# Kernel tuning notes

Measured on AMD Instinct MI355X. Metric: run time of the kernel, lower is better.

The kernel has to match this reference:

```python
import jax, jax.numpy as jnp
import numpy as np

EMBED_CHOICES = (512, 768, 1024)
RATIO_CHOICES = (2, 3, 4)
D_MAX = 1024           # max embed_dim
H_MAX = 4096           # max expansion dim = 1024 * 4


def setup_inputs() -> dict:
    key = jax.random.key(0)
    ks = jax.random.split(key, 7)
    return {
        "x": jax.random.normal(ks[0], (8, 512, D_MAX), dtype=jnp.float32),
        "w0": jax.random.normal(ks[1], (H_MAX, D_MAX), dtype=jnp.float32) * 0.02,
        "b0": jax.random.normal(ks[2], (H_MAX,), dtype=jnp.float32) * 0.02,
        "w1": jax.random.normal(ks[3], (D_MAX, H_MAX), dtype=jnp.float32) * 0.02,
        "b1": jax.random.normal(ks[4], (D_MAX,), dtype=jnp.float32) * 0.02,
        "arch_embed": jax.random.normal(ks[5], (3,), dtype=jnp.float32),
        "arch_mlp": jax.random.normal(ks[6], (3,), dtype=jnp.float32),
    }


def _effective_masks(a, b):
    """Weighted-sum-of-sliced-linears == single linear with masked effective weights.

    Candidate (e, r): uses W0[:e*r, :e] on x[..., :e], zero-padded to H_MAX,
    and W1[:e, :e*r] on h[..., :e*r], zero-padded to D_MAX.
    """
    col = jnp.arange(D_MAX)
    row = jnp.arange(H_MAX)
    m0 = jnp.zeros((H_MAX, D_MAX), dtype=jnp.float32)
    bm0 = jnp.zeros((H_MAX,), dtype=jnp.float32)
    m1 = jnp.zeros((D_MAX, H_MAX), dtype=jnp.float32)
    bm1 = jnp.zeros((D_MAX,), dtype=jnp.float32)
    for ie, e in enumerate(EMBED_CHOICES):
        cm = (col < e).astype(jnp.float32)          # [D_MAX]
        for ir, r in enumerate(RATIO_CHOICES):
            w = a[ie] * b[ir]
            rm = (row < e * r).astype(jnp.float32)  # [H_MAX]
            m0 = m0 + w * rm[:, None] * cm[None, :]
            bm0 = bm0 + w * rm
            m1 = m1 + w * cm[:, None] * rm[None, :]
            bm1 = bm1 + w * cm
    return m0, bm0, m1, bm1


def reference(x, w0, b0, w1, b1, arch_embed, arch_mlp):
    a = jax.nn.softmax(arch_embed)  # DARTS-style arch weights over embed_dim
    b = jax.nn.softmax(arch_mlp)    # over mlp_ratio
    m0, bm0, m1, bm1 = _effective_masks(a, b)
    # layer 0 mix: [B,S,D] @ [D,H] -> [B,S,H]
    h = jnp.einsum("bsd,hd->bsh", x, m0 * w0) + bm0 * b0
    h = jax.nn.relu(h)
    # layer 1 mix: [B,S,H] @ [H,D] -> [B,S,D]
    out = jnp.einsum("bsh,dh->bsd", h, m1 * w1) + bm1 * b1
    # dropout p=0.0 (eval): identity
    return out
```

## Files before the change

### kernel.cpp

```cpp
#include <hip/hip_runtime.h>


typedef __attribute__((ext_vector_type(8))) short bf16x8;
typedef __attribute__((ext_vector_type(4))) float f32x4;
typedef __attribute__((ext_vector_type(8))) unsigned short u16x8;

__device__ __forceinline__ unsigned short f2bf(float f) {
  unsigned int x = __float_as_uint(f);
  x += 0x7fffu + ((x >> 16) & 1u);
  return (unsigned short)(x >> 16);
}

__device__ __forceinline__ void softmax3(const float* __restrict__ p, float* o) {
  float m = fmaxf(p[0], fmaxf(p[1], p[2]));
  float e0 = expf(p[0] - m), e1 = expf(p[1] - m), e2 = expf(p[2] - m);
  float inv = 1.0f / (e0 + e1 + e2);
  o[0] = e0 * inv; o[1] = e1 * inv; o[2] = e2 * inv;
}

__device__ __forceinline__ float sval(int h, int d, const float a[3], const float b[3]) {
  constexpr int E[3] = {512, 768, 1024};
  constexpr int R[3] = {2, 3, 4};
  float s = 0.f;
#pragma unroll
  for (int ie = 0; ie < 3; ++ie) {
    if (d < E[ie]) {
      float t = 0.f;
#pragma unroll
      for (int ir = 0; ir < 3; ++ir)
        if (h < E[ie] * R[ir]) t += b[ir];
      s += a[ie] * t;
    }
  }
  return s;
}


__device__ __forceinline__ void cvt8(const float* __restrict__ src,
                                     unsigned short* __restrict__ dst,
                                     size_t base, float s) {
  const f32x4* p = (const f32x4*)(src + base);
  f32x4 v0 = p[0], v1 = p[1];
  u16x8 r;
#pragma unroll
  for (int j = 0; j < 4; ++j) { r[j] = f2bf(v0[j] * s); r[4 + j] = f2bf(v1[j] * s); }
  *(u16x8*)(dst + base) = r;
}

__global__ __launch_bounds__(256) void conv_all(const float* __restrict__ x,
                                                const float* __restrict__ w0,
                                                const float* __restrict__ b0,
                                                const float* __restrict__ w1,
                                                const float* __restrict__ b1,
                                                const float* __restrict__ ae,
                                                const float* __restrict__ am,
                                                unsigned short* __restrict__ xb,
                                                unsigned short* __restrict__ w0e,
                                                unsigned short* __restrict__ w1e,
                                                float* __restrict__ bb0,
                                                float* __restrict__ bb1) {
  int t = blockIdx.x * 256 + threadIdx.x;
  float a[3], b[3];
  softmax3(ae, a); softmax3(am, b);
  if (t < 524288) {
    cvt8(x, xb, (size_t)t * 8, 1.0f);
  } else if (t < 1048576) {
    int base = (t - 524288) * 8;
    cvt8(w0, w0e, base, sval(base >> 10, base & 1023, a, b));
  } else if (t < 1572864) {
    int base = (t - 1048576) * 8;
    cvt8(w1, w1e, base, sval(base & 4095, base >> 12, a, b));
  } else if (t < 1573504) {
    int base = (t - 1572864) * 8;
#pragma unroll
    for (int j = 0; j < 8; ++j) {
      int i = base + j;
      if (i < 4096) bb0[i] = sval(i, 0, a, b) * b0[i];
      else          bb1[i - 4096] = sval(0, i - 4096, a, b) * b1[i - 4096];
    }
  }
}


template <int MODE>
__device__ __forceinline__ void gemm_core(const unsigned short* __restrict__ A,
                                          const unsigned short* __restrict__ B,
                                          const float* __restrict__ bias,
                                          void* __restrict__ Cout,
                                          int M, int N, int K, int Ksub) {
  __shared__ unsigned short As[2][128 * 64];
  __shared__ unsigned short Bs[2][128 * 64];

  const int tid  = threadIdx.x;
  const int lane = tid & 63;
  const int w    = tid >> 6;
  const int m0   = blockIdx.x * 128;
  const int n0   = blockIdx.y * 128;
  const int wm   = (w >> 1) * 64;
  const int wn   = (w & 1) * 64;
  const int kbeg = (MODE == 2) ? blockIdx.z * Ksub : 0;
  const int nt   = Ksub >> 6;

  f32x4 acc[4][4] = {};

  const int srow = tid >> 3;
  const int scol = (tid & 7) * 8;
  const unsigned short* Ag = A + (size_t)(m0 + srow) * K + scol;
  const unsigned short* Bg = B + (size_t)(n0 + srow) * K + scol;

  auto stage = [&](int buf, int k0) {
#pragma unroll
    for (int i = 0; i < 4; ++i) {
      __builtin_amdgcn_global_load_lds(
          (const __attribute__((address_space(1))) void*)(Ag + (size_t)(i * 32) * K + k0),
          (__attribute__((address_space(3))) void*)(&As[buf][0] + tid * 8 + i * 2048), 16, 0, 0);
      __builtin_amdgcn_global_load_lds(
          (const __attribute__((address_space(1))) void*)(Bg + (size_t)(i * 32) * K + k0),
          (__attribute__((address_space(3))) void*)(&Bs[buf][0] + tid * 8 + i * 2048), 16, 0, 0);
    }
  };

  stage(0, kbeg);
  int cur = 0;
  for (int t = 0; t < nt; ++t) {
    const int k0 = kbeg + t * 64;
    if (t + 1 < nt) {
      stage(cur ^ 1, k0 + 64);
      asm volatile("s_waitcnt vmcnt(8)" ::: "memory");
    } else {
      asm volatile("s_waitcnt vmcnt(0)" ::: "memory");
    }
    __builtin_amdgcn_s_barrier();
    asm volatile("" ::: "memory");

#pragma unroll
    for (int ks = 0; ks < 2; ++ks) {
      const int ko = ks * 32 + (lane >> 4) * 8;
      bf16x8 af[4], bfr[4];
#pragma unroll
      for (int m = 0; m < 4; ++m)
        af[m] = *(const bf16x8*)&As[cur][(wm + m * 16 + (lane & 15)) * 64 + ko];
#pragma unroll
      for (int n = 0; n < 4; ++n)
        bfr[n] = *(const bf16x8*)&Bs[cur][(wn + n * 16 + (lane & 15)) * 64 + ko];
#pragma unroll
      for (int m = 0; m < 4; ++m)
#pragma unroll
        for (int n = 0; n < 4; ++n)
          acc[m][n] = __builtin_amdgcn_mfma_f32_16x16x32_bf16(af[m], bfr[n], acc[m][n], 0, 0, 0);
    }

    asm volatile("s_waitcnt lgkmcnt(0)" ::: "memory");
    __builtin_amdgcn_s_barrier();
    cur ^= 1;
  }

  const int crow = (lane >> 4) * 4;
  const int ccol = lane & 15;
#pragma unroll
  for (int m = 0; m < 4; ++m) {
#pragma unroll
    for (int n = 0; n < 4; ++n) {
      const int gr = m0 + wm + m * 16 + crow;
      const int gc = n0 + wn + n * 16 + ccol;
      if (MODE == 0) {
        const float bv = bias[gc];
        unsigned short* H = (unsigned short*)Cout;
#pragma unroll
        for (int r = 0; r < 4; ++r) {
          float v = fmaxf(acc[m][n][r] + bv, 0.f);
          H[(size_t)(gr + r) * N + gc] = f2bf(v);
        }
      } else if (MODE == 1) {
        const float bv = bias[gc];
        float* C = (float*)Cout;
#pragma unroll
        for (int r = 0; r < 4; ++r)
          C[(size_t)(gr + r) * N + gc] = acc[m][n][r] + bv;
      } else {
        float* P = (float*)Cout + (size_t)blockIdx.z * M * N;
#pragma unroll
        for (int r = 0; r < 4; ++r)
          P[(size_t)(gr + r) * N + gc] = acc[m][n][r];
      }
    }
  }
}

__global__ __launch_bounds__(256) void gemm_h(const unsigned short* __restrict__ A,
                                              const unsigned short* __restrict__ B,
                                              const float* __restrict__ bias,
                                              void* __restrict__ C,
                                              int M, int N, int K, int Ksub) {
  gemm_core<0>(A, B, bias, C, M, N, K, Ksub);
}
__global__ __launch_bounds__(256) void gemm_f(const unsigned short* __restrict__ A,
                                              const unsigned short* __restrict__ B,
                                              const float* __restrict__ bias,
                                              void* __restrict__ C,
                                              int M, int N, int K, int Ksub) {
  gemm_core<1>(A, B, bias, C, M, N, K, Ksub);
}
__global__ __launch_bounds__(256) void gemm_p(const unsigned short* __restrict__ A,
                                              const unsigned short* __restrict__ B,
                                              const float* __restrict__ bias,
                                              void* __restrict__ C,
                                              int M, int N, int K, int Ksub) {
  gemm_core<2>(A, B, bias, C, M, N, K, Ksub);
}

__global__ __launch_bounds__(256) void reduce_k(const float* __restrict__ P,
                                                const float* __restrict__ bb1,
                                                float* __restrict__ out,
                                                int n4) {
  const f32x4* p = (const f32x4*)P;
  const f32x4* bv = (const f32x4*)bb1;
  f32x4* o = (f32x4*)out;
  for (int i = blockIdx.x * 256 + threadIdx.x; i < n4; i += gridDim.x * 256) {
    f32x4 v = p[i];
    v += p[i + n4];
    v += p[i + 2 * n4];
    v += p[i + 3 * n4];
    v += bv[i & 255];
    o[i] = v;
  }
}


extern "C" void kernel_launch(void* const* d_in, const int* in_sizes, int n_in,
                              void* d_out, int out_size, void* d_ws, size_t ws_size,
                              hipStream_t stream) {
  const float* x  = (const float*)d_in[0];
  const float* w0 = (const float*)d_in[1];
  const float* b0 = (const float*)d_in[2];
  const float* w1 = (const float*)d_in[3];
  const float* b1 = (const float*)d_in[4];
  const float* ae = (const float*)d_in[5];
  const float* am = (const float*)d_in[6];

  char* ws = (char*)d_ws;
  unsigned short* xb   = (unsigned short*)(ws);
  unsigned short* w0e  = (unsigned short*)(ws + (8u  << 20));
  unsigned short* w1e  = (unsigned short*)(ws + (16u << 20));
  unsigned short* Hbuf = (unsigned short*)(ws + (24u << 20));
  float* bb0 = (float*)(ws + (56u << 20));
  float* bb1 = (float*)(ws + (56u << 20) + 16384);
  float* part = (float*)(ws + (57u << 20));
  const size_t WS_NEEDED = (57u << 20) + (64u << 20);

  conv_all<<<6147, 256, 0, stream>>>(x, w0, b0, w1, b1, ae, am,
                                     xb, w0e, w1e, bb0, bb1);

  dim3 g1(32, 32);
  gemm_h<<<g1, 256, 0, stream>>>(xb, w0e, bb0, Hbuf, 4096, 4096, 1024, 1024);

  if (ws_size >= WS_NEEDED) {
    dim3 g2(32, 8, 4);
    gemm_p<<<g2, 256, 0, stream>>>(Hbuf, w1e, nullptr, part, 4096, 1024, 4096, 1024);
    reduce_k<<<2048, 256, 0, stream>>>(part, bb1, (float*)d_out, 1024 * 1024);
  } else {
    dim3 g2(32, 8);
    gemm_f<<<g2, 256, 0, stream>>>(Hbuf, w1e, bb1, d_out, 4096, 1024, 4096, 4096);
  }
}
```

Baseline: 217.3 us.

## Rewrite GEMMs as 256x256 tiles with 8 waves, swizzled LDS and interleaved prefetch

Replaces the 128x128, 4-wave GEMM kernel with a 256x256 tile kernel using 512 threads and 128KB of dynamic LDS. Each K-tile is split into two 32-wide halves, the LDS layout is XOR-swizzled to avoid bank conflicts, and the next tile's global-to-LDS loads are interleaved between MFMA groups, with s_setprio raised around the MFMA blocks. The goal is more data reuse per loaded byte and better overlap of loads with compute. In exchange the grids shrink (256 blocks for the first GEMM, 256 for the split-K second GEMM), so wave-level occupancy and tail balance across CUs may suffer, and register pressure rises to 128 accumulators per thread.

Result: faster. 189.2 us (-12.9%).

```diff
diff --git a/kernel.cpp b/kernel.cpp
--- a/kernel.cpp
+++ b/kernel.cpp
@@ -4,6 +4,9 @@
 typedef __attribute__((ext_vector_type(8))) short bf16x8;
 typedef __attribute__((ext_vector_type(4))) float f32x4;
 typedef __attribute__((ext_vector_type(8))) unsigned short u16x8;
+
+#define AS1 __attribute__((address_space(1)))
+#define AS3 __attribute__((address_space(3)))
 
 __device__ __forceinline__ unsigned short f2bf(float f) {
   unsigned int x = __float_as_uint(f);
@@ -83,92 +86,136 @@
 
 
 template <int MODE>
-__device__ __forceinline__ void gemm_core(const unsigned short* __restrict__ A,
-                                          const unsigned short* __restrict__ B,
-                                          const float* __restrict__ bias,
-                                          void* __restrict__ Cout,
-                                          int M, int N, int K, int Ksub) {
-  __shared__ unsigned short As[2][128 * 64];
-  __shared__ unsigned short Bs[2][128 * 64];
+__global__ __launch_bounds__(512, 2) void gemm256(const unsigned short* __restrict__ A,
+                                                  const unsigned short* __restrict__ B,
+                                                  const float* __restrict__ bias,
+                                                  void* __restrict__ Cout,
+                                                  int M, int N, int K, int Ksub) {
+  extern __shared__ unsigned short lds[];
 
   const int tid  = threadIdx.x;
   const int lane = tid & 63;
-  const int w    = tid >> 6;
-  const int m0   = blockIdx.x * 128;
-  const int n0   = blockIdx.y * 128;
-  const int wm   = (w >> 1) * 64;
-  const int wn   = (w & 1) * 64;
+  const int wid  = tid >> 6;
+  const int m0   = blockIdx.x * 256;
+  const int n0   = blockIdx.y * 256;
+  const int wm   = (wid >> 2) * 128;
+  const int wn   = (wid & 3) * 64;
   const int kbeg = (MODE == 2) ? blockIdx.z * Ksub : 0;
   const int nt   = Ksub >> 6;
 
-  f32x4 acc[4][4] = {};
-
-  const int srow = tid >> 3;
-  const int scol = (tid & 7) * 8;
-  const unsigned short* Ag = A + (size_t)(m0 + srow) * K + scol;
-  const unsigned short* Bg = B + (size_t)(n0 + srow) * K + scol;
-
-  auto stage = [&](int buf, int k0) {
-#pragma unroll
-    for (int i = 0; i < 4; ++i) {
-      __builtin_amdgcn_global_load_lds(
-          (const __attribute__((address_space(1))) void*)(Ag + (size_t)(i * 32) * K + k0),
-          (__attribute__((address_space(3))) void*)(&As[buf][0] + tid * 8 + i * 2048), 16, 0, 0);
-      __builtin_amdgcn_global_load_lds(
-          (const __attribute__((address_space(1))) void*)(Bg + (size_t)(i * 32) * K + k0),
-          (__attribute__((address_space(3))) void*)(&Bs[buf][0] + tid * 8 + i * 2048), 16, 0, 0);
-    }
+  f32x4 acc[8][4] = {};
+
+  const int srow   = tid >> 2;
+  const int schunk = (tid & 3) ^ ((tid >> 3) & 3);
+  const unsigned short* Ag = A + (size_t)(m0 + srow) * K + schunk * 8;
+  const unsigned short* Bg = B + (size_t)(n0 + srow) * K + schunk * 8;
+  const size_t rstep = (size_t)128 * K;
+
+  auto stageA = [&](int buf, int h, int k) {
+    unsigned short* d = lds + (buf * 2 + h) * 8192 + tid * 8;
+    __builtin_amdgcn_global_load_lds((const AS1 void*)(Ag + k + h * 32),
+                                     (AS3 void*)d, 16, 0, 0);
+    __builtin_amdgcn_global_load_lds((const AS1 void*)(Ag + rstep + k + h * 32),
+                                     (AS3 void*)(d + 4096), 16, 0, 0);
   };
-
-  stage(0, kbeg);
-  int cur = 0;
-  for (int t = 0; t < nt; ++t) {
-    const int k0 = kbeg + t * 64;
-    if (t + 1 < nt) {
-      stage(cur ^ 1, k0 + 64);
-      asm volatile("s_waitcnt vmcnt(8)" ::: "memory");
-    } else {
-      asm volatile("s_waitcnt vmcnt(0)" ::: "memory");
-    }
+  auto stageB = [&](int buf, int h, int k) {
+    unsigned short* d = lds + 32768 + (buf * 2 + h) * 8192 + tid * 8;
+    __builtin_amdgcn_global_load_lds((const AS1 void*)(Bg + k + h * 32),
+                                     (AS3 void*)d, 16, 0, 0);
+    __builtin_amdgcn_global_load_lds((const AS1 void*)(Bg + rstep + k + h * 32),
+                                     (AS3 void*)(d + 4096), 16, 0, 0);
+  };
+
+  const int rc = ((lane >> 4) * 8) ^ (((lane >> 1) & 3) << 3);
+  const int ra = (lane & 15) * 32 + rc;
+
+  stageA(0, 0, kbeg); stageB(0, 0, kbeg);
+  stageA(0, 1, kbeg); stageB(0, 1, kbeg);
+
+  int buf = 0;
+  for (int T = 0; T < nt; ++T) {
+    const int kn = kbeg + T * 64 + 64;
+    const bool pf = (T + 1 < nt);
+    bf16x8 af[4], bfr[4];
+    const int ab = (buf * 2) * 8192;
+    const int bb = 32768 + (buf * 2) * 8192;
+
+    asm volatile("s_waitcnt vmcnt(4)" ::: "memory");
     __builtin_amdgcn_s_barrier();
     asm volatile("" ::: "memory");
-
-#pragma unroll
-    for (int ks = 0; ks < 2; ++ks) {
-      const int ko = ks * 32 + (lane >> 4) * 8;
-      bf16x8 af[4], bfr[4];
-#pragma unroll
-      for (int m = 0; m < 4; ++m)
-        af[m] = *(const bf16x8*)&As[cur][(wm + m * 16 + (lane & 15)) * 64 + ko];
-#pragma unroll
-      for (int n = 0; n < 4; ++n)
-        bfr[n] = *(const bf16x8*)&Bs[cur][(wn + n * 16 + (lane & 15)) * 64 + ko];
-#pragma unroll
-      for (int m = 0; m < 4; ++m)
-#pragma unroll
-        for (int n = 0; n < 4; ++n)
-          acc[m][n] = __builtin_amdgcn_mfma_f32_16x16x32_bf16(af[m], bfr[n], acc[m][n], 0, 0, 0);
-    }
-
-    asm volatile("s_waitcnt lgkmcnt(0)" ::: "memory");
+    if (pf) stageA(buf ^ 1, 0, kn);
+#pragma unroll
+    for (int n = 0; n < 4; ++n)
+      bfr[n] = *(const bf16x8*)&lds[bb + (wn + n * 16) * 32 + ra];
+#pragma unroll
+    for (int m = 0; m < 4; ++m)
+      af[m] = *(const bf16x8*)&lds[ab + (wm + m * 16) * 32 + ra];
+    __builtin_amdgcn_s_setprio(1);
+#pragma unroll
+    for (int m = 0; m < 4; ++m)
+#pragma unroll
+      for (int n = 0; n < 4; ++n)
+        acc[m][n] = __builtin_amdgcn_mfma_f32_16x16x32_bf16(af[m], bfr[n], acc[m][n], 0, 0, 0);
+    __builtin_amdgcn_s_setprio(0);
+    if (pf) stageB(buf ^ 1, 0, kn);
+#pragma unroll
+    for (int m = 0; m < 4; ++m)
+      af[m] = *(const bf16x8*)&lds[ab + (wm + 64 + m * 16) * 32 + ra];
+    __builtin_amdgcn_s_setprio(1);
+#pragma unroll
+    for (int m = 0; m < 4; ++m)
+#pragma unroll
+      for (int n = 0; n < 4; ++n)
+        acc[4 + m][n] = __builtin_amdgcn_mfma_f32_16x16x32_bf16(af[m], bfr[n], acc[4 + m][n], 0, 0, 0);
+    __builtin_amdgcn_s_setprio(0);
+
+    if (pf) { asm volatile("s_waitcnt vmcnt(4)" ::: "memory"); }
+    else    { asm volatile("s_waitcnt vmcnt(0)" ::: "memory"); }
     __builtin_amdgcn_s_barrier();
-    cur ^= 1;
+    asm volatile("" ::: "memory");
+    if (pf) stageA(buf ^ 1, 1, kn);
+#pragma unroll
+    for (int n = 0; n < 4; ++n)
+      bfr[n] = *(const bf16x8*)&lds[bb + 8192 + (wn + n * 16) * 32 + ra];
+#pragma unroll
+    for (int m = 0; m < 4; ++m)
+      af[m] = *(const bf16x8*)&lds[ab + 8192 + (wm + m * 16) * 32 + ra];
+    __builtin_amdgcn_s_setprio(1);
+#pragma unroll
+    for (int m = 0; m < 4; ++m)
+#pragma unroll
+      for (int n = 0; n < 4; ++n)
+        acc[m][n] = __builtin_amdgcn_mfma_f32_16x16x32_bf16(af[m], bfr[n], acc[m][n], 0, 0, 0);
+    __builtin_amdgcn_s_setprio(0);
+    if (pf) stageB(buf ^ 1, 1, kn);
+#pragma unroll
+    for (int m = 0; m < 4; ++m)
+      af[m] = *(const bf16x8*)&lds[ab + 8192 + (wm + 64 + m * 16) * 32 + ra];
+    __builtin_amdgcn_s_setprio(1);
+#pragma unroll
+    for (int m = 0; m < 4; ++m)
+#pragma unroll
+      for (int n = 0; n < 4; ++n)
+        acc[4 + m][n] = __builtin_amdgcn_mfma_f32_16x16x32_bf16(af[m], bfr[n], acc[4 + m][n], 0, 0, 0);
+    __builtin_amdgcn_s_setprio(0);
+
+    buf ^= 1;
   }
 
   const int crow = (lane >> 4) * 4;
   const int ccol = lane & 15;
 #pragma unroll
-  for (int m = 0; m < 4; ++m) {
+  for (int mi = 0; mi < 8; ++mi) {
 #pragma unroll
     for (int n = 0; n < 4; ++n) {
-      const int gr = m0 + wm + m * 16 + crow;
+      const int gr = m0 + wm + mi * 16 + crow;
       const int gc = n0 + wn + n * 16 + ccol;
       if (MODE == 0) {
         const float bv = bias[gc];
         unsigned short* H = (unsigned short*)Cout;
 #pragma unroll
         for (int r = 0; r < 4; ++r) {
-          float v = fmaxf(acc[m][n][r] + bv, 0.f);
+          float v = fmaxf(acc[mi][n][r] + bv, 0.f);
           H[(size_t)(gr + r) * N + gc] = f2bf(v);
         }
       } else if (MODE == 1) {
@@ -176,37 +223,15 @@
         float* C = (float*)Cout;
 #pragma unroll
         for (int r = 0; r < 4; ++r)
-          C[(size_t)(gr + r) * N + gc] = acc[m][n][r] + bv;
+          C[(size_t)(gr + r) * N + gc] = acc[mi][n][r] + bv;
       } else {
         float* P = (float*)Cout + (size_t)blockIdx.z * M * N;
 #pragma unroll
         for (int r = 0; r < 4; ++r)
-          P[(size_t)(gr + r) * N + gc] = acc[m][n][r];
+          P[(size_t)(gr + r) * N + gc] = acc[mi][n][r];
       }
     }
   }
-}
-
-__global__ __launch_bounds__(256) void gemm_h(const unsigned short* __restrict__ A,
-                                              const unsigned short* __restrict__ B,
-                                              const float* __restrict__ bias,
-                                              void* __restrict__ C,
-                                              int M, int N, int K, int Ksub) {
-  gemm_core<0>(A, B, bias, C, M, N, K, Ksub);
-}
-__global__ __launch_bounds__(256) void gemm_f(const unsigned short* __restrict__ A,
-                                              const unsigned short* __restrict__ B,
-                                              const float* __restrict__ bias,
-                                              void* __restrict__ C,
-                                              int M, int N, int K, int Ksub) {
-  gemm_core<1>(A, B, bias, C, M, N, K, Ksub);
-}
-__global__ __launch_bounds__(256) void gemm_p(const unsigned short* __restrict__ A,
-                                              const unsigned short* __restrict__ B,
-                                              const float* __restrict__ bias,
-                                              void* __restrict__ C,
-                                              int M, int N, int K, int Ksub) {
-  gemm_core<2>(A, B, bias, C, M, N, K, Ksub);
 }
 
 __global__ __launch_bounds__(256) void reduce_k(const float* __restrict__ P,
@@ -251,15 +276,15 @@
   conv_all<<<6147, 256, 0, stream>>>(x, w0, b0, w1, b1, ae, am,
                                      xb, w0e, w1e, bb0, bb1);
 
-  dim3 g1(32, 32);
-  gemm_h<<<g1, 256, 0, stream>>>(xb, w0e, bb0, Hbuf, 4096, 4096, 1024, 1024);
+  dim3 g1(16, 16);
+  gemm256<0><<<g1, 512, 131072, stream>>>(xb, w0e, bb0, Hbuf, 4096, 4096, 1024, 1024);
 
   if (ws_size >= WS_NEEDED) {
-    dim3 g2(32, 8, 4);
-    gemm_p<<<g2, 256, 0, stream>>>(Hbuf, w1e, nullptr, part, 4096, 1024, 4096, 1024);
+    dim3 g2(16, 4, 4);
+    gemm256<2><<<g2, 512, 131072, stream>>>(Hbuf, w1e, nullptr, part, 4096, 1024, 4096, 1024);
     reduce_k<<<2048, 256, 0, stream>>>(part, bb1, (float*)d_out, 1024 * 1024);
   } else {
-    dim3 g2(32, 8);
-    gemm_f<<<g2, 256, 0, stream>>>(Hbuf, w1e, bb1, d_out, 4096, 1024, 4096, 4096);
-  }
-}
+    dim3 g2(16, 4);
+    gemm256<1><<<g2, 512, 131072, stream>>>(Hbuf, w1e, bb1, d_out, 4096, 1024, 4096, 4096);
+  }
+}
```
